# Kernel optimization log

Measured on AMD Instinct MI355X. Metric: run time of the kernel, lower is better.

The kernel has to match this reference:

```python
import jax, jax.numpy as jnp
import numpy as np

EMBED_DIM = 1024
NUM_HEADS = 16
HEAD_DIM = EMBED_DIM // NUM_HEADS
B, S = 2, 2048
NEG = -1e20


def setup_inputs() -> dict:
    key = jax.random.key(0)
    ks = jax.random.split(key, 8)
    scale = 0.02
    return {
        "query": jax.random.normal(ks[0], (B, S, EMBED_DIM), jnp.float32),
        "keys": jax.random.normal(ks[1], (B, S, EMBED_DIM), jnp.float32),
        "values": jax.random.normal(ks[2], (B, S, EMBED_DIM), jnp.float32),
        "mask": jax.random.randint(ks[3], (1, 1, S, S), 0, 2, jnp.int32),
        "Wq": jax.random.normal(ks[4], (EMBED_DIM, EMBED_DIM), jnp.float32) * scale,
        "Wk": jax.random.normal(ks[5], (EMBED_DIM, EMBED_DIM), jnp.float32) * scale,
        "Wv": jax.random.normal(ks[6], (EMBED_DIM, EMBED_DIM), jnp.float32) * scale,
        "Wo": jax.random.normal(ks[7], (EMBED_DIM, EMBED_DIM), jnp.float32) * scale,
        "bo": jnp.zeros((EMBED_DIM,), jnp.float32),
    }


def reference(query, keys, values, mask, Wq, Wk, Wv, Wo, bo):
    N, Lq, _ = query.shape
    Lk = keys.shape[1]
    # torch nn.Linear: y = x @ W.T  (bias=False for Q/K/V)
    Q = (query @ Wq.T).reshape(N, Lq, NUM_HEADS, HEAD_DIM)
    K = (keys @ Wk.T).reshape(N, Lk, NUM_HEADS, HEAD_DIM)
    V = (values @ Wv.T).reshape(N, Lk, NUM_HEADS, HEAD_DIM)
    # NOTE: source scales by sqrt(embed_dim), not sqrt(head_dim) — kept faithful.
    energy = jnp.einsum("nqhd,nkhd->nhqk", Q, K) / jnp.sqrt(
        jnp.asarray(EMBED_DIM, Q.dtype)
    )
    energy = jnp.where(mask == 0, jnp.asarray(NEG, energy.dtype), energy)
    attention = jax.nn.softmax(energy, axis=3)
    out = jnp.einsum("nhqk,nkhd->nqhd", attention, V).reshape(N, Lq, EMBED_DIM)
    return out @ Wo.T + bo
```

## Files before the change

kernel.cpp:

```cpp
#include <hip/hip_runtime.h>
#include <stdint.h>

typedef __bf16 bf16;
typedef __bf16 bf16x4 __attribute__((ext_vector_type(4)));
typedef __bf16 bf16x8 __attribute__((ext_vector_type(8)));
typedef float f32x4 __attribute__((ext_vector_type(4)));
typedef float f32x16 __attribute__((ext_vector_type(16)));

#define MFMA16(a, b, c) __builtin_amdgcn_mfma_f32_16x16x32_bf16((a), (b), (c), 0, 0, 0)
#define MFMA32(a, b, c) __builtin_amdgcn_mfma_f32_32x32x16_bf16((a), (b), (c), 0, 0, 0)

__device__ __forceinline__ void gload16(const bf16* g, bf16* l) {
    __builtin_amdgcn_global_load_lds(
        (const __attribute__((address_space(1))) void*)g,
        (__attribute__((address_space(3))) void*)l, 16, 0, 0);
}

__global__ __launch_bounds__(256) void cvt_kernel(
    const float* __restrict__ q, const float* __restrict__ k, const float* __restrict__ v,
    const float* __restrict__ wq, const float* __restrict__ wk,
    const float* __restrict__ wv, const float* __restrict__ wo,
    bf16* __restrict__ qb, bf16* __restrict__ kb, bf16* __restrict__ vb,
    bf16* __restrict__ wqb, bf16* __restrict__ wkb, bf16* __restrict__ wvb,
    bf16* __restrict__ wob)
{
    int z = blockIdx.z;
    const float* src; bf16* dst; int n;
    switch (z) {
        case 0:  src = q;  dst = qb;  n = 4194304; break;
        case 1:  src = k;  dst = kb;  n = 4194304; break;
        case 2:  src = v;  dst = vb;  n = 4194304; break;
        case 3:  src = wq; dst = wqb; n = 1048576; break;
        case 4:  src = wk; dst = wkb; n = 1048576; break;
        case 5:  src = wv; dst = wvb; n = 1048576; break;
        default: src = wo; dst = wob; n = 1048576; break;
    }
    int i = (blockIdx.x * 256 + threadIdx.x) * 8;
    if (i >= n) return;
    float4 f0 = *(const float4*)(src + i);
    float4 f1 = *(const float4*)(src + i + 4);
    bf16x8 o;
    o[0] = (bf16)f0.x; o[1] = (bf16)f0.y; o[2] = (bf16)f0.z; o[3] = (bf16)f0.w;
    o[4] = (bf16)f1.x; o[5] = (bf16)f1.y; o[6] = (bf16)f1.z; o[7] = (bf16)f1.w;
    *(bf16x8*)(dst + i) = o;
}

__global__ __launch_bounds__(256) void maskpack_kernel(
    const int* __restrict__ mask, unsigned long long* __restrict__ maskb)
{
    int gid  = blockIdx.x * 256 + threadIdx.x;
    int word = gid >> 6;
    int lane = gid & 63;
    int row = word >> 5, wc = word & 31;
    int mv = mask[row * 2048 + wc * 64 + lane];
    unsigned long long bits = __ballot(mv != 0);
    if (lane == 0) maskb[word] = bits;
}

template <int OUTMODE, int MT>
__global__ __launch_bounds__(256) void gemm_kernel(
    const bf16* __restrict__ A0, const bf16* __restrict__ A1, const bf16* __restrict__ A2,
    const bf16* __restrict__ B0, const bf16* __restrict__ B1, const bf16* __restrict__ B2,
    bf16* __restrict__ C0, bf16* __restrict__ C1, bf16* __restrict__ C2,
    const float* __restrict__ bias, float* __restrict__ outf)
{
    constexpr int MI = (MT == 128) ? 4 : 2;

    const int z = blockIdx.z;
    const bf16* A = (z == 0) ? A0 : (z == 1) ? A1 : A2;
    const bf16* B = (z == 0) ? B0 : (z == 1) ? B1 : B2;

    __shared__ bf16 At[MT * 32];
    __shared__ bf16 Bt[128 * 32];

    const int tid  = threadIdx.x;
    const int lane = tid & 63;
    const int wave = tid >> 6;
    const int quad = lane >> 4;
    const int l16  = lane & 15;
    const int wm = (wave >> 1) * (MT / 2);
    const int wn = (wave & 1) * 64;
    const int m0 = blockIdx.y * MT;
    const int n0 = blockIdx.x * 128;

    const int lrow = lane >> 2;
    const int lcol = (lane & 3) * 8;

    f32x4 acc[MI][4] = {};

    const bf16* Ag = A + (size_t)(m0 + lrow) * 1024 + lcol;
    const bf16* Bg = B + (size_t)(n0 + lrow) * 1024 + lcol;

    for (int k0 = 0; k0 < 1024; k0 += 32) {
        __syncthreads();
        if constexpr (MT == 128) {
#pragma unroll
            for (int j = 0; j < 2; ++j)
                gload16(Ag + (size_t)(wave * 32 + j * 16) * 1024 + k0,
                        At + (wave * 32 + j * 16) * 32);
        } else {
            gload16(Ag + (size_t)(wave * 16) * 1024 + k0, At + (wave * 16) * 32);
        }
#pragma unroll
        for (int j = 0; j < 2; ++j)
            gload16(Bg + (size_t)(wave * 32 + j * 16) * 1024 + k0,
                    Bt + (wave * 32 + j * 16) * 32);
        __syncthreads();

        bf16x8 af[MI], bg[4];
#pragma unroll
        for (int i = 0; i < MI; ++i)
            af[i] = *(const bf16x8*)(At + (wm + i * 16 + l16) * 32 + quad * 8);
#pragma unroll
        for (int j = 0; j < 4; ++j)
            bg[j] = *(const bf16x8*)(Bt + (wn + j * 16 + l16) * 32 + quad * 8);
#pragma unroll
        for (int i = 0; i < MI; ++i)
#pragma unroll
            for (int j = 0; j < 4; ++j)
                acc[i][j] = MFMA16(af[i], bg[j], acc[i][j]);
    }

    if constexpr (OUTMODE == 0) {
        bf16* C = (z == 0) ? C0 : (z == 1) ? C1 : C2;
        const float cs = (z == 0) ? 0.03125f : 1.0f;
#pragma unroll
        for (int i = 0; i < MI; ++i)
#pragma unroll
            for (int j = 0; j < 4; ++j) {
                int row = m0 + wm + i * 16 + quad * 4;
                int col = n0 + wn + j * 16 + l16;
#pragma unroll
                for (int r = 0; r < 4; ++r)
                    C[(row + r) * 1024 + col] = (bf16)(acc[i][j][r] * cs);
            }
    } else {
#pragma unroll
        for (int j = 0; j < 4; ++j) {
            int col = n0 + wn + j * 16 + l16;
            float bj = bias[col];
#pragma unroll
            for (int i = 0; i < MI; ++i) {
                int row = m0 + wm + i * 16 + quad * 4;
#pragma unroll
                for (int r = 0; r < 4; ++r)
                    outf[(row + r) * 1024 + col] = acc[i][j][r] + bj;
            }
        }
    }
}

__global__ __launch_bounds__(256) void transpose_kernel(const bf16* __restrict__ V,
                                                        bf16* __restrict__ Vt)
{
    __shared__ bf16 t[64][72];
    const int tid = threadIdx.x;
    const int b  = blockIdx.z;
    const int s0 = blockIdx.x * 64;
    const int d0 = blockIdx.y * 64;
#pragma unroll
    for (int c = 0; c < 2; ++c) {
        int qq = c * 256 + tid;
        int row = qq >> 3, col = (qq & 7) * 8;
        *(uint4*)(&t[row][col]) =
            *(const uint4*)(V + (size_t)(b * 2048 + s0 + row) * 1024 + d0 + col);
    }
    __syncthreads();
#pragma unroll
    for (int c = 0; c < 2; ++c) {
        int qq = c * 256 + tid;
        int drow = qq >> 3, scol = (qq & 7) * 8;
        bf16x8 o;
#pragma unroll
        for (int j = 0; j < 8; ++j) o[j] = t[scol + j][drow];
        *(bf16x8*)(Vt + (size_t)(b * 1024 + d0 + drow) * 2048 + s0 + scol) = o;
    }
}

__global__ __launch_bounds__(256) void flash_kernel(
    const bf16* __restrict__ Q, const bf16* __restrict__ K, const bf16* __restrict__ Vt,
    const unsigned long long* __restrict__ maskb, bf16* __restrict__ O)
{
    __shared__ bf16 Kl[64 * 64];
    __shared__ bf16 Vl[64 * 64];
    __shared__ bf16 Pl[128 * 72];

    const int tid  = threadIdx.x;
    const int lane = tid & 63;
    const int wave = tid >> 6;
    const int l32  = lane & 31;
    const int hl   = lane >> 5;
    const int l7   = lane & 7;
    const int b  = blockIdx.z;
    const int h  = blockIdx.y;
    const int q0 = blockIdx.x * 128;
    const int qt = q0 + wave * 32;

    const bf16* Qb = Q + (size_t)(b * 2048 + qt + l32) * 1024 + h * 64 + hl * 8;
    bf16x8 qf[4];
#pragma unroll
    for (int ks = 0; ks < 4; ++ks) qf[ks] = *(const bf16x8*)(Qb + ks * 16);

    bf16x8 ones;
#pragma unroll
    for (int j = 0; j < 8; ++j) ones[j] = (bf16)1.0f;

    f32x16 acc[2] = {};
    f32x16 lacc = {};

    const int dmarow = lane >> 3;
    const int dmacol = (l7 ^ dmarow) * 8;
    const bf16* Kg = K + (size_t)(b * 2048 + wave * 16 + dmarow) * 1024 + h * 64 + dmacol;
    const bf16* Vg = Vt + (size_t)((b * 16 + h) * 64 + wave * 16 + dmarow) * 2048 + dmacol;
    bf16* Kw = Kl + (wave * 16) * 64;
    bf16* Vw = Vl + (wave * 16) * 64;
    const unsigned long long* Mg = maskb + (size_t)(qt + l32) * 32;

    bf16* Pq = Pl + (wave * 32 + l32) * 72;

    for (int kt = 0; kt < 2048; kt += 64) {
        unsigned long long mw = Mg[kt >> 6];
        __syncthreads();
        gload16(Kg + (size_t)kt * 1024,       Kw);
        gload16(Kg + (size_t)(kt + 8) * 1024, Kw + 8 * 64);
        gload16(Vg + kt,                      Vw);
        gload16(Vg + kt + 8 * 2048,           Vw + 8 * 64);
        __syncthreads();

#pragma unroll
        for (int t = 0; t < 2; ++t) {
            f32x16 s = {};
#pragma unroll
            for (int ks = 0; ks < 4; ++ks) {
                bf16x8 ka = *(const bf16x8*)(Kl + (t * 32 + l32) * 64 +
                                             (((ks * 2 + hl) ^ l7) * 8));
                s = MFMA32(ka, qf[ks], s);
            }
            unsigned long long mwt = mw >> (t * 32 + 4 * hl);
#pragma unroll
            for (int g = 0; g < 4; ++g) {
                bf16x4 pv;
#pragma unroll
                for (int r = 0; r < 4; ++r) {
                    bool keep = (mwt >> (8 * g + r)) & 1ULL;
                    float e = __expf(s[g * 4 + r]);
                    pv[r] = keep ? (bf16)e : (bf16)0.0f;
                }
                *(bf16x4*)(Pq + t * 32 + 4 * hl + 8 * g) = pv;
            }
        }

        bf16x8 pa[4];
#pragma unroll
        for (int ks = 0; ks < 4; ++ks)
            pa[ks] = *(const bf16x8*)(Pq + ks * 16 + hl * 8);
#pragma unroll
        for (int dt = 0; dt < 2; ++dt)
#pragma unroll
            for (int ks = 0; ks < 4; ++ks) {
                bf16x8 vb = *(const bf16x8*)(Vl + (dt * 32 + l32) * 64 +
                                             (((ks * 2 + hl) ^ l7) * 8));
                acc[dt] = MFMA32(pa[ks], vb, acc[dt]);
            }
#pragma unroll
        for (int ks = 0; ks < 4; ++ks)
            lacc = MFMA32(pa[ks], ones, lacc);
    }

    const size_t obase = (size_t)(b * 2048 + qt) * 1024 + h * 64;
#pragma unroll
    for (int g = 0; g < 4; ++g)
#pragma unroll
        for (int r = 0; r < 4; ++r) {
            int qr = 4 * hl + 8 * g + r;
            float inv = 1.0f / lacc[g * 4 + r];
            O[obase + (size_t)qr * 1024 + l32]      = (bf16)(acc[0][g * 4 + r] * inv);
            O[obase + (size_t)qr * 1024 + 32 + l32] = (bf16)(acc[1][g * 4 + r] * inv);
        }
}

extern "C" void kernel_launch(void* const* d_in, const int* in_sizes, int n_in,
                              void* d_out, int out_size, void* d_ws, size_t ws_size,
                              hipStream_t stream)
{
    const float* q  = (const float*)d_in[0];
    const float* k  = (const float*)d_in[1];
    const float* v  = (const float*)d_in[2];
    const int* mask = (const int*)d_in[3];
    const float* wq = (const float*)d_in[4];
    const float* wk = (const float*)d_in[5];
    const float* wv = (const float*)d_in[6];
    const float* wo = (const float*)d_in[7];
    const float* bo = (const float*)d_in[8];
    float* out = (float*)d_out;

    char* p = (char*)d_ws;
    auto alloc = [&](size_t bytes) {
        char* r = p;
        p += (bytes + 255) & ~(size_t)255;
        return r;
    };
    const size_t SB = (size_t)4096 * 1024 * 2;
    const size_t WB = (size_t)1024 * 1024 * 2;
    bf16* qb  = (bf16*)alloc(SB);
    bf16* kb  = (bf16*)alloc(SB);
    bf16* vb  = (bf16*)alloc(SB);
    bf16* wqb = (bf16*)alloc(WB);
    bf16* wkb = (bf16*)alloc(WB);
    bf16* wvb = (bf16*)alloc(WB);
    bf16* wob = (bf16*)alloc(WB);
    bf16* Qp  = (bf16*)alloc(SB);
    bf16* Kp  = (bf16*)alloc(SB);
    bf16* Vp  = (bf16*)alloc(SB);
    bf16* Vtp = (bf16*)alloc(SB);
    bf16* Ob  = (bf16*)alloc(SB);
    unsigned long long* maskb = (unsigned long long*)alloc(2048 * 32 * 8);

    cvt_kernel<<<dim3(2048, 1, 7), 256, 0, stream>>>(
        q, k, v, wq, wk, wv, wo, qb, kb, vb, wqb, wkb, wvb, wob);

    maskpack_kernel<<<dim3(16384), 256, 0, stream>>>(mask, maskb);

    gemm_kernel<0, 128><<<dim3(8, 32, 3), 256, 0, stream>>>(
        qb, kb, vb, wqb, wkb, wvb, Qp, Kp, Vp, nullptr, nullptr);

    transpose_kernel<<<dim3(32, 16, 2), 256, 0, stream>>>(Vp, Vtp);

    flash_kernel<<<dim3(16, 16, 2), 256, 0, stream>>>(Qp, Kp, Vtp, maskb, Ob);

    gemm_kernel<1, 64><<<dim3(8, 64, 1), 256, 0, stream>>>(
        Ob, nullptr, nullptr, wob, nullptr, nullptr,
        nullptr, nullptr, nullptr, bo, out);
}
```

Before: 259.3 us.

## Double-buffer K/V tiles and keep P in registers via lane shuffles

The flash attention loop now double-buffers the K and V tiles in LDS. The next tile's async global-to-LDS loads are issued right after a single barrier, so they overlap with the current tile's MFMA work. The P tile no longer round-trips through shared memory: each lane packs its bf16 probabilities and swaps halves with the partner lane through cross-lane shuffles, forming the MFMA A operand directly. The exponent switches to a hardware exp2 with log2(e) folded into the Q scaling factor. The cost is twice the K/V LDS footprint and reliance on the barrier waiting for the outstanding LDS-DMA loads.

```diff
diff --git a/kernel.cpp b/kernel.cpp
--- a/kernel.cpp
+++ b/kernel.cpp
@@ -6,6 +6,8 @@
 typedef __bf16 bf16x8 __attribute__((ext_vector_type(8)));
 typedef float f32x4 __attribute__((ext_vector_type(4)));
 typedef float f32x16 __attribute__((ext_vector_type(16)));
+typedef unsigned int uintx2 __attribute__((ext_vector_type(2)));
+typedef unsigned int uintx4 __attribute__((ext_vector_type(4)));
 
 #define MFMA16(a, b, c) __builtin_amdgcn_mfma_f32_16x16x32_bf16((a), (b), (c), 0, 0, 0)
 #define MFMA32(a, b, c) __builtin_amdgcn_mfma_f32_32x32x16_bf16((a), (b), (c), 0, 0, 0)
@@ -14,6 +16,14 @@
     __builtin_amdgcn_global_load_lds(
         (const __attribute__((address_space(1))) void*)g,
         (__attribute__((address_space(3))) void*)l, 16, 0, 0);
+}
+
+__device__ __forceinline__ float fast_exp2(float x) {
+#if __has_builtin(__builtin_amdgcn_exp2f)
+    return __builtin_amdgcn_exp2f(x);
+#else
+    return exp2f(x);
+#endif
 }
 
 __global__ __launch_bounds__(256) void cvt_kernel(
@@ -123,7 +133,7 @@
 
     if constexpr (OUTMODE == 0) {
         bf16* C = (z == 0) ? C0 : (z == 1) ? C1 : C2;
-        const float cs = (z == 0) ? 0.03125f : 1.0f;
+        const float cs = (z == 0) ? 0.0450842200277800f : 1.0f;
 #pragma unroll
         for (int i = 0; i < MI; ++i)
 #pragma unroll
@@ -181,9 +191,8 @@
     const bf16* __restrict__ Q, const bf16* __restrict__ K, const bf16* __restrict__ Vt,
     const unsigned long long* __restrict__ maskb, bf16* __restrict__ O)
 {
-    __shared__ bf16 Kl[64 * 64];
-    __shared__ bf16 Vl[64 * 64];
-    __shared__ bf16 Pl[128 * 72];
+    __shared__ bf16 Kl[2][64 * 64];
+    __shared__ bf16 Vl[2][64 * 64];
 
     const int tid  = threadIdx.x;
     const int lane = tid & 63;
@@ -212,59 +221,83 @@
     const int dmacol = (l7 ^ dmarow) * 8;
     const bf16* Kg = K + (size_t)(b * 2048 + wave * 16 + dmarow) * 1024 + h * 64 + dmacol;
     const bf16* Vg = Vt + (size_t)((b * 16 + h) * 64 + wave * 16 + dmarow) * 2048 + dmacol;
-    bf16* Kw = Kl + (wave * 16) * 64;
-    bf16* Vw = Vl + (wave * 16) * 64;
     const unsigned long long* Mg = maskb + (size_t)(qt + l32) * 32;
 
-    bf16* Pq = Pl + (wave * 32 + l32) * 72;
-
-    for (int kt = 0; kt < 2048; kt += 64) {
-        unsigned long long mw = Mg[kt >> 6];
+    auto stage = [&](bf16* Kd, bf16* Vd, int kt) {
+        gload16(Kg + (size_t)kt * 1024,       Kd + (wave * 16) * 64);
+        gload16(Kg + (size_t)(kt + 8) * 1024, Kd + (wave * 16 + 8) * 64);
+        gload16(Vg + kt,                      Vd + (wave * 16) * 64);
+        gload16(Vg + kt + 8 * 2048,           Vd + (wave * 16 + 8) * 64);
+    };
+
+    unsigned long long mw = Mg[0];
+    stage(Kl[0], Vl[0], 0);
+
+    auto body = [&](const bf16* Kc, const bf16* Vc, bf16* Kn, bf16* Vn, int it) {
         __syncthreads();
-        gload16(Kg + (size_t)kt * 1024,       Kw);
-        gload16(Kg + (size_t)(kt + 8) * 1024, Kw + 8 * 64);
-        gload16(Vg + kt,                      Vw);
-        gload16(Vg + kt + 8 * 2048,           Vw + 8 * 64);
-        __syncthreads();
-
+        unsigned long long mw_next = 0;
+        if (it + 1 < 32) {
+            stage(Kn, Vn, (it + 1) * 64);
+            mw_next = Mg[it + 1];
+        }
+
+        bf16x8 pa[4];
 #pragma unroll
         for (int t = 0; t < 2; ++t) {
             f32x16 s = {};
 #pragma unroll
             for (int ks = 0; ks < 4; ++ks) {
-                bf16x8 ka = *(const bf16x8*)(Kl + (t * 32 + l32) * 64 +
+                bf16x8 ka = *(const bf16x8*)(Kc + (t * 32 + l32) * 64 +
                                              (((ks * 2 + hl) ^ l7) * 8));
                 s = MFMA32(ka, qf[ks], s);
             }
-            unsigned long long mwt = mw >> (t * 32 + 4 * hl);
+            unsigned mwt = (unsigned)(mw >> (t * 32 + 4 * hl));
+            unsigned W[4][2];
 #pragma unroll
             for (int g = 0; g < 4; ++g) {
                 bf16x4 pv;
 #pragma unroll
                 for (int r = 0; r < 4; ++r) {
-                    bool keep = (mwt >> (8 * g + r)) & 1ULL;
-                    float e = __expf(s[g * 4 + r]);
-                    pv[r] = keep ? (bf16)e : (bf16)0.0f;
+                    float ev = fast_exp2(s[g * 4 + r]);
+                    pv[r] = (mwt & (1u << (8 * g + r))) ? (bf16)ev : (bf16)0.0f;
                 }
-                *(bf16x4*)(Pq + t * 32 + 4 * hl + 8 * g) = pv;
-            }
-        }
-
-        bf16x8 pa[4];
-#pragma unroll
-        for (int ks = 0; ks < 4; ++ks)
-            pa[ks] = *(const bf16x8*)(Pq + ks * 16 + hl * 8);
+                uintx2 u = __builtin_bit_cast(uintx2, pv);
+                W[g][0] = u[0];
+                W[g][1] = u[1];
+            }
+#pragma unroll
+            for (int kh = 0; kh < 2; ++kh) {
+                unsigned s0 = hl ? W[2 * kh][0] : W[2 * kh + 1][0];
+                unsigned s1 = hl ? W[2 * kh][1] : W[2 * kh + 1][1];
+                unsigned r0 = __shfl_xor(s0, 32, 64);
+                unsigned r1 = __shfl_xor(s1, 32, 64);
+                uintx4 aw;
+                aw[0] = hl ? r0 : W[2 * kh][0];
+                aw[1] = hl ? r1 : W[2 * kh][1];
+                aw[2] = hl ? W[2 * kh + 1][0] : r0;
+                aw[3] = hl ? W[2 * kh + 1][1] : r1;
+                pa[t * 2 + kh] = __builtin_bit_cast(bf16x8, aw);
+            }
+        }
+
 #pragma unroll
         for (int dt = 0; dt < 2; ++dt)
 #pragma unroll
             for (int ks = 0; ks < 4; ++ks) {
-                bf16x8 vb = *(const bf16x8*)(Vl + (dt * 32 + l32) * 64 +
+                bf16x8 vb = *(const bf16x8*)(Vc + (dt * 32 + l32) * 64 +
                                              (((ks * 2 + hl) ^ l7) * 8));
                 acc[dt] = MFMA32(pa[ks], vb, acc[dt]);
             }
 #pragma unroll
         for (int ks = 0; ks < 4; ++ks)
             lacc = MFMA32(pa[ks], ones, lacc);
+
+        mw = mw_next;
+    };
+
+    for (int it = 0; it < 32; it += 2) {
+        body(Kl[0], Vl[0], Kl[1], Vl[1], it);
+        body(Kl[1], Vl[1], Kl[0], Vl[0], it + 1);
     }
 
     const size_t obase = (size_t)(b * 2048 + qt) * 1024 + h * 64;
```

After: 255.9 us. No clear change (-1.3%).
